# Performance work log

Hardware: AMD Instinct MI355X
Metric: run time of the kernel (lower is better)

The kernel has to match this reference:

```python
import jax, jax.numpy as jnp
import numpy as np

# Static problem sizes
B, TMAX = 32, 48                 # subjects, max windows per subject
NPW, NWIN = 128, 1024            # nodes per window, total windows (= sum(lengths))
EPW = 2048                       # edges per window (avg degree 16)
N, E = NWIN * NPW, NWIN * EPW    # 131072 nodes, 2097152 edges
IN_DIM, GNN_H, GRU_H = 128, 128, 128


def setup_inputs() -> dict:
    key = jax.random.key(0)
    ks = jax.random.split(key, 12)
    x = jax.random.normal(ks[0], (N, IN_DIM), jnp.float32)
    # random intra-window edges: endpoints within each window's 128-node block
    base = jax.random.randint(ks[1], (2, NWIN, EPW), 0, NPW)
    offs = (jnp.arange(NWIN) * NPW)[None, :, None]
    edge_index = (base + offs).reshape(2, E)
    batch_idx = jnp.repeat(jnp.arange(NWIN), NPW)          # node -> window id
    lengths = jnp.asarray(np.tile([16, 48], B // 2), jnp.int32)  # sums to NWIN
    s = 0.05
    p = lambda k, shape: jax.random.normal(k, shape, jnp.float32) * s
    return dict(
        x=x, edge_index=edge_index, batch_idx=batch_idx, lengths=lengths,
        # GIN layer 1 MLP (weights stored [in,out])
        w1a=p(ks[2], (IN_DIM, GNN_H)), b1a=jnp.zeros((GNN_H,), jnp.float32),
        w1b=p(ks[3], (GNN_H, GNN_H)), b1b=jnp.zeros((GNN_H,), jnp.float32),
        # GIN layer 2 MLP
        w2a=p(ks[4], (GNN_H, GNN_H)), b2a=jnp.zeros((GNN_H,), jnp.float32),
        w2b=p(ks[5], (GNN_H, GNN_H)), b2b=jnp.zeros((GNN_H,), jnp.float32),
        # GRU (torch layout: [3H, in], gate order r,z,n)
        wih=p(ks[6], (3 * GRU_H, GNN_H)), whh=p(ks[7], (3 * GRU_H, GRU_H)),
        bih=jnp.zeros((3 * GRU_H,), jnp.float32), bhh=jnp.zeros((3 * GRU_H,), jnp.float32),
        # output head
        wout=p(ks[8], (GRU_H, 1)), bout=jnp.zeros((1,), jnp.float32),
    )


def _gin(h, src, dst, wa, ba, wb, bb):
    # GINConv with eps=0: mlp(x + sum_{j->i} x_j)
    aggr = jax.ops.segment_sum(h[src], dst, num_segments=N)
    z = h + aggr
    z = jax.nn.relu(z @ wa + ba)
    return z @ wb + bb


def _forward(x, w1a, b1a, w1b, b1b, w2a, b2a, w2b, b2b,
             wih, whh, bih, bhh, wout, bout, edge_index, batch_idx, lengths):
    src, dst = edge_index[0], edge_index[1]
    h = jax.nn.relu(_gin(x, src, dst, w1a, b1a, w1b, b1b))
    h = jax.nn.relu(_gin(h, src, dst, w2a, b2a, w2b, b2b))
    # global mean pool per window -> [NWIN, GNN_H]
    sums = jax.ops.segment_sum(h, batch_idx, num_segments=NWIN)
    cnt = jax.ops.segment_sum(jnp.ones((N, 1), h.dtype), batch_idx, num_segments=NWIN)
    g = sums / cnt
    # pad_sequence: scatter flat window embeddings into [B, TMAX, H]
    csum = jnp.cumsum(lengths)
    starts = jnp.concatenate([jnp.zeros((1,), lengths.dtype), csum[:-1]])
    win_ids = jnp.arange(NWIN)
    subj = jnp.searchsorted(csum, win_ids, side='right')
    pos = win_ids - starts[subj]
    padded = jnp.zeros((B, TMAX, GNN_H), g.dtype).at[subj, pos].set(g)
    # masked GRU == pack_padded_sequence semantics (state frozen past length)
    mask = jnp.arange(TMAX)[:, None] < lengths[None, :]   # [T, B]
    xs = jnp.swapaxes(padded, 0, 1)                        # [T, B, H]

    def step(hc, inputs):
        xt, mt = inputs
        gx = xt @ wih.T + bih
        gh = hc @ whh.T + bhh
        rx, zx, nx = jnp.split(gx, 3, axis=-1)
        rh, zh, nh = jnp.split(gh, 3, axis=-1)
        r = jax.nn.sigmoid(rx + rh)
        z = jax.nn.sigmoid(zx + zh)
        n = jnp.tanh(nx + r * nh)
        hn = (1 - z) * n + z * hc
        hn = jnp.where(mt[:, None], hn, hc)
        return hn, None

    h0 = jnp.zeros((B, GRU_H), g.dtype)
    h_last, _ = jax.lax.scan(step, h0, (xs, mask))
    return (h_last @ wout + bout).squeeze(-1)  # [B]


def reference(x, edge_index, batch_idx, lengths,
              w1a, b1a, w1b, b1b, w2a, b2a, w2b, b2b,
              wih, whh, bih, bhh, wout, bout):
    return _forward(x, w1a, b1a, w1b, b1b, w2a, b2a, w2b, b2b,
                    wih, whh, bih, bhh, wout, bout, edge_index, batch_idx, lengths)
```

## Files before the change

### kernel.cpp

```cpp
#include <hip/hip_runtime.h>
#include <hip/hip_bf16.h>
#include <stdint.h>

#define NPW   128
#define NWIN  1024
#define EPW   2048
#define NEDGE (NWIN * EPW)
#define BSUBJ 32
#define TMAXW 48

typedef __bf16 bf16x8_t __attribute__((ext_vector_type(8)));
typedef float  f32x4_t  __attribute__((ext_vector_type(4)));

#define MU4_OFF  0
#define B2_OFF   8192
#define B3_OFF   40960
#define BIAS_OFF 73728
#define GP_OFF   75776
#define META_OFF 76288
#define K1_LDS   76800

__device__ __forceinline__ unsigned short bfbits(float v) {
  return __builtin_bit_cast(unsigned short, (__bf16)v);
}
__device__ __forceinline__ int swz(int row, int colbyte) {
  return row * 256 + (colbyte ^ ((row & 15) << 4));
}

#define GLDS16(gaddr, laddr) __builtin_amdgcn_global_load_lds( \
    (const __attribute__((address_space(1))) unsigned*)(gaddr), \
    (__attribute__((address_space(3))) unsigned*)(laddr), 16, 0, 0)

__device__ __forceinline__ void wstage(const char* src, char* dstB3, int wv, int lane) {
  #pragma unroll
  for (int p = 0; p < 4; ++p)
    GLDS16(src + wv * 4096 + p * 1024 + lane * 16, dstB3 + wv * 4096 + p * 1024);
}

__device__ __forceinline__ void gemm_lds(const char* Ab, const char* Bb, int lane, int rt,
                                         f32x4_t acc[8]) {
  const int rowA = rt * 16 + (lane & 15);
  const int swA = (rowA & 15) << 4;
  const int swB = (lane & 15) << 4;
  #pragma unroll
  for (int kk = 0; kk < 4; ++kk) {
    const int kb = kk * 64 + (lane >> 4) * 16;
    bf16x8_t af = *(const bf16x8_t*)(Ab + rowA * 256 + (kb ^ swA));
    #pragma unroll
    for (int ct = 0; ct < 8; ++ct) {
      const int rowB = ct * 16 + (lane & 15);
      bf16x8_t bv = *(const bf16x8_t*)(Bb + rowB * 256 + (kb ^ swB));
      acc[ct] = __builtin_amdgcn_mfma_f32_16x16x32_bf16(af, bv, acc[ct], 0, 0, 0);
    }
  }
}

__device__ __forceinline__ void gemm_m(const unsigned* Mw, const char* Bb, int lane, int rt,
                                       f32x4_t acc[8]) {
  const int rowA = rt * 16 + (lane & 15);
  const int g = lane >> 4;
  const int swB = (lane & 15) << 4;
  #pragma unroll
  for (int kk = 0; kk < 4; ++kk) {
    const unsigned mw = Mw[rowA * 16 + ((kk * 4 + g) ^ (rowA & 15))];
    bf16x8_t af;
    #pragma unroll
    for (int e = 0; e < 8; ++e)
      af[e] = (__bf16)(float)((mw >> (4 * e)) & 15u);
    const int kb = kk * 64 + g * 16;
    #pragma unroll
    for (int ct = 0; ct < 8; ++ct) {
      const int rowB = ct * 16 + (lane & 15);
      bf16x8_t bv = *(const bf16x8_t*)(Bb + rowB * 256 + (kb ^ swB));
      acc[ct] = __builtin_amdgcn_mfma_f32_16x16x32_bf16(af, bv, acc[ct], 0, 0, 0);
    }
  }
}

__device__ __forceinline__ void write_row(char* Dst, int lane, int rt, const f32x4_t acc[8],
                                          const float* bias, bool relu) {
  const int r0 = rt * 16 + (lane >> 4) * 4;
  const int c = lane & 15;
  #pragma unroll
  for (int ct = 0; ct < 8; ++ct) {
    const int col = ct * 16 + c;
    const float bvl = bias ? bias[col] : 0.f;
    #pragma unroll
    for (int j = 0; j < 4; ++j) {
      float v = acc[ct][j] + bvl;
      if (relu) v = fmaxf(v, 0.f);
      *(__bf16*)(Dst + swz(r0 + j, col * 2)) = (__bf16)v;
    }
  }
}

__device__ __forceinline__ void write_tr(char* Dst, int lane, int rt, const f32x4_t acc[8],
                                         const float* bias, bool relu) {
  const int r0 = rt * 16 + (lane >> 4) * 4;
  const int c = lane & 15;
  #pragma unroll
  for (int ct = 0; ct < 8; ++ct) {
    const int col = ct * 16 + c;
    const float bvl = bias ? bias[col] : 0.f;
    unsigned long long pk = 0ull;
    #pragma unroll
    for (int j = 0; j < 4; ++j) {
      float v = acc[ct][j] + bvl;
      if (relu) v = fmaxf(v, 0.f);
      pk |= ((unsigned long long)bfbits(v)) << (16 * j);
    }
    *(unsigned long long*)(Dst + swz(col, r0 * 2)) = pk;
  }
}

__global__ void __launch_bounds__(128)
wprep_kernel(const float* __restrict__ w1a, const float* __restrict__ w1b,
             const float* __restrict__ w2a, const float* __restrict__ w2b,
             unsigned* __restrict__ wt) {
  const float* srcs[4] = {w1a, w1b, w2a, w2b};
  const float* src = srcs[blockIdx.x];
  const int j = threadIdx.x;
  unsigned* dst = wt + blockIdx.x * 8192 + j * 64;
  const int sw = (j & 15) << 2;
  #pragma unroll 8
  for (int k = 0; k < 64; ++k) {
    float a = src[(size_t)(2 * k) * 128 + j];
    float b = src[(size_t)(2 * k + 1) * 128 + j];
    dst[k ^ sw] = (unsigned)bfbits(a) | ((unsigned)bfbits(b) << 16);
  }
}

__global__ void __launch_bounds__(512, 2)
gin_gnn_kernel(const float* __restrict__ x, const int* __restrict__ ei,
               const float* __restrict__ b1a, const float* __restrict__ b1b,
               const float* __restrict__ b2a, const float* __restrict__ b2b,
               const char* __restrict__ wt_sw, const float* __restrict__ wih,
               const float* __restrict__ bih, const int* __restrict__ lengths,
               float* __restrict__ GX) {
  extern __shared__ __align__(16) char sm[];
  const int w = blockIdx.x;
  const int tid = threadIdx.x;
  const int lane = tid & 63;
  const int wv = tid >> 6;

  unsigned* Mw = (unsigned*)(sm + MU4_OFF);
  char* B2 = sm + B2_OFF;
  char* B3 = sm + B3_OFF;
  float* biasb = (float*)(sm + BIAS_OFF);
  float* gp = (float*)(sm + GP_OFF);
  int* meta = (int*)(sm + META_OFF);

  #pragma unroll
  for (int i = tid; i < 2048; i += 512) Mw[i] = 0u;
  if (tid < 128) gp[tid] = 0.f;
  __syncthreads();

  wstage(wt_sw, B3, wv, lane);
  if (tid < 64) {
    int L = (tid < BSUBJ) ? lengths[tid] : 0;
    int c = L;
    #pragma unroll
    for (int d = 1; d < 32; d <<= 1) {
      int u = __shfl_up(c, d, 64);
      if (tid >= d) c += u;
    }
    unsigned long long mset = __ballot(tid < BSUBJ && w < c);
    int s = (int)(__ffsll((long long)mset) - 1);
    if (tid == s) { meta[0] = s; meta[1] = w - (c - L); }
  }
  {
    const int base = w * EPW;
    #pragma unroll
    for (int rr = 0; rr < 4; ++rr) {
      const int e = base + tid + rr * 512;
      const int s = ei[e] & 127;
      const int d = ei[NEDGE + e] & 127;
      atomicAdd(&Mw[d * 16 + ((s >> 3) ^ (d & 15))], 1u << ((s & 7) * 4));
    }
    if (tid < 128) {
      const int d = tid;
      atomicAdd(&Mw[d * 16 + ((d >> 3) ^ (d & 15))], 1u << ((d & 7) * 4));
    }
  }
  {
    const float* xw = x + (size_t)w * 16384;
    #pragma unroll
    for (int it = 0; it < 8; ++it) {
      const int elem = it * 2048 + tid * 4;
      const float4 v = *(const float4*)(xw + elem);
      const int row = elem >> 7;
      const int colb = (elem & 127) * 2;
      unsigned long long pk = (unsigned long long)bfbits(v.x)
          | ((unsigned long long)bfbits(v.y) << 16)
          | ((unsigned long long)bfbits(v.z) << 32)
          | ((unsigned long long)bfbits(v.w) << 48);
      *(unsigned long long*)(B2 + row * 256 + (colb ^ ((row & 15) << 4))) = pk;
    }
  }
  {
    const float* bp = (tid < 128) ? b1a : (tid < 256) ? b1b : (tid < 384) ? b2a : b2b;
    biasb[tid] = bp[tid & 127];
  }
  __syncthreads();

  f32x4_t acc[8];
  #define ZACC() { _Pragma("unroll") for (int q = 0; q < 8; ++q) acc[q] = (f32x4_t){0.f,0.f,0.f,0.f}; }

  ZACC(); gemm_lds(B2, B3, lane, wv, acc);
  __syncthreads();
  write_tr(B2, lane, wv, acc, nullptr, false);
  wstage(wt_sw + 32768, B3, wv, lane);
  __syncthreads();
  ZACC(); gemm_m(Mw, B2, lane, wv, acc);
  __syncthreads();
  write_row(B2, lane, wv, acc, biasb + 0, true);
  __syncthreads();
  ZACC(); gemm_lds(B2, B3, lane, wv, acc);
  __syncthreads();
  write_row(B2, lane, wv, acc, biasb + 128, true);
  wstage(wt_sw + 65536, B3, wv, lane);
  __syncthreads();
  ZACC(); gemm_lds(B2, B3, lane, wv, acc);
  __syncthreads();
  write_tr(B2, lane, wv, acc, nullptr, false);
  wstage(wt_sw + 98304, B3, wv, lane);
  __syncthreads();
  ZACC(); gemm_m(Mw, B2, lane, wv, acc);
  __syncthreads();
  write_row(B2, lane, wv, acc, biasb + 256, true);
  __syncthreads();
  ZACC(); gemm_lds(B2, B3, lane, wv, acc);
  {
    const int c = lane & 15;
    #pragma unroll
    for (int ct = 0; ct < 8; ++ct) {
      const int col = ct * 16 + c;
      const float bvl = biasb[384 + col];
      float s = 0.f;
      #pragma unroll
      for (int j = 0; j < 4; ++j) s += fmaxf(acc[ct][j] + bvl, 0.f);
      s += __shfl_xor(s, 16);
      s += __shfl_xor(s, 32);
      if (lane < 16) atomicAdd(&gp[col], s);
    }
  }
  __syncthreads();

  if (tid < 384) {
    const float* wrow = wih + (size_t)tid * 128;
    const float4* gp4 = (const float4*)gp;
    float a0 = 0.f, a1 = 0.f, a2 = 0.f, a3 = 0.f;
    #pragma unroll
    for (int q = 0; q < 8; ++q) {
      const float4 h0 = gp4[4*q], h1 = gp4[4*q+1], h2 = gp4[4*q+2], h3 = gp4[4*q+3];
      const float4 w0 = *(const float4*)(wrow + 16*q);
      const float4 w1 = *(const float4*)(wrow + 16*q + 4);
      const float4 w2 = *(const float4*)(wrow + 16*q + 8);
      const float4 w3 = *(const float4*)(wrow + 16*q + 12);
      a0 = fmaf(w0.x,h0.x,fmaf(w0.y,h0.y,fmaf(w0.z,h0.z,fmaf(w0.w,h0.w,a0))));
      a1 = fmaf(w1.x,h1.x,fmaf(w1.y,h1.y,fmaf(w1.z,h1.z,fmaf(w1.w,h1.w,a1))));
      a2 = fmaf(w2.x,h2.x,fmaf(w2.y,h2.y,fmaf(w2.z,h2.z,fmaf(w2.w,h2.w,a2))));
      a3 = fmaf(w3.x,h3.x,fmaf(w3.y,h3.y,fmaf(w3.z,h3.z,fmaf(w3.w,h3.w,a3))));
    }
    const float dot = (a0 + a1) + (a2 + a3);
    GX[((size_t)meta[0] * TMAXW + meta[1]) * 384 + tid] = dot * (1.f / 128.f) + bih[tid];
  }
}

__global__ void __launch_bounds__(384)
gru_kernel(const float* __restrict__ GX, const float* __restrict__ whh,
           const float* __restrict__ bhh, const float* __restrict__ wout,
           const float* __restrict__ bout, const int* __restrict__ lengths,
           float* __restrict__ outp) {
  __shared__ __align__(16) float hb[128];
  __shared__ float rb[128], zb[128];
  const int b = blockIdx.x;
  const int o = threadIdx.x;

  float wrf[128];
  {
    const float* wr = whh + (size_t)o * 128;
    #pragma unroll
    for (int q = 0; q < 32; ++q) {
      float4 v = ((const float4*)wr)[q];
      wrf[4*q+0] = v.x; wrf[4*q+1] = v.y; wrf[4*q+2] = v.z; wrf[4*q+3] = v.w;
    }
  }
  if (o < 128) hb[o] = 0.f;
  const float bho = bhh[o];
  const int len = lengths[b];
  __syncthreads();

  float gx = (len > 0) ? GX[((size_t)b * TMAXW) * 384 + o] : 0.f;
  for (int t = 0; t < len; ++t) {
    const int tn = (t + 1 < len) ? t + 1 : t;
    const float gxn = GX[((size_t)b * TMAXW + tn) * 384 + o];
    float a0 = 0.f, a1 = 0.f, a2 = 0.f, a3 = 0.f;
    const float4* hv4 = (const float4*)hb;
    #pragma unroll
    for (int q = 0; q < 8; ++q) {
      const float4 h0 = hv4[4*q], h1 = hv4[4*q+1], h2 = hv4[4*q+2], h3 = hv4[4*q+3];
      const float* wq = wrf + 16 * q;
      a0 = fmaf(wq[0],  h0.x, a0); a0 = fmaf(wq[1],  h0.y, a0);
      a0 = fmaf(wq[2],  h0.z, a0); a0 = fmaf(wq[3],  h0.w, a0);
      a1 = fmaf(wq[4],  h1.x, a1); a1 = fmaf(wq[5],  h1.y, a1);
      a1 = fmaf(wq[6],  h1.z, a1); a1 = fmaf(wq[7],  h1.w, a1);
      a2 = fmaf(wq[8],  h2.x, a2); a2 = fmaf(wq[9],  h2.y, a2);
      a2 = fmaf(wq[10], h2.z, a2); a2 = fmaf(wq[11], h2.w, a2);
      a3 = fmaf(wq[12], h3.x, a3); a3 = fmaf(wq[13], h3.y, a3);
      a3 = fmaf(wq[14], h3.z, a3); a3 = fmaf(wq[15], h3.w, a3);
    }
    const float gh = (a0 + a1) + (a2 + a3) + bho;
    float nsave = 0.f, ghn = 0.f;
    if (o < 256) {
      const float v = 1.f / (1.f + __expf(-(gx + gh)));
      if (o < 128) rb[o] = v; else zb[o - 128] = v;
    } else {
      nsave = gx; ghn = gh;
    }
    __syncthreads();
    if (o >= 256) {
      const int oo = o - 256;
      const float r = rb[oo], z = zb[oo];
      const float pre = nsave + r * ghn;
      const float e2 = __expf(-2.f * pre);
      const float n = (1.f - e2) / (1.f + e2);
      hb[oo] = (1.f - z) * n + z * hb[oo];
    }
    __syncthreads();
    gx = gxn;
  }

  float part = (o < 128) ? hb[o] * wout[o] : 0.f;
  #pragma unroll
  for (int d = 1; d < 64; d <<= 1) part += __shfl_xor(part, d);
  __shared__ float red[6];
  if ((o & 63) == 0) red[o >> 6] = part;
  __syncthreads();
  if (o == 0) outp[b] = red[0] + red[1] + bout[0];
}

extern "C" void kernel_launch(void* const* d_in, const int* in_sizes, int n_in,
                              void* d_out, int out_size, void* d_ws, size_t ws_size,
                              hipStream_t stream) {
  const float* x    = (const float*)d_in[0];
  const int*   ei   = (const int*)d_in[1];
  const int*   len  = (const int*)d_in[3];
  const float* w1a  = (const float*)d_in[4];
  const float* b1a  = (const float*)d_in[5];
  const float* w1b  = (const float*)d_in[6];
  const float* b1b  = (const float*)d_in[7];
  const float* w2a  = (const float*)d_in[8];
  const float* b2a  = (const float*)d_in[9];
  const float* w2b  = (const float*)d_in[10];
  const float* b2b  = (const float*)d_in[11];
  const float* wih  = (const float*)d_in[12];
  const float* whh  = (const float*)d_in[13];
  const float* bih  = (const float*)d_in[14];
  const float* bhh  = (const float*)d_in[15];
  const float* wout = (const float*)d_in[16];
  const float* bout = (const float*)d_in[17];

  float*    GX    = (float*)d_ws;
  unsigned* wt_sw = (unsigned*)((char*)d_ws + (size_t)BSUBJ * TMAXW * 384 * 4);

  hipLaunchKernelGGL(wprep_kernel, dim3(4), dim3(128), 0, stream,
                     w1a, w1b, w2a, w2b, wt_sw);
  hipLaunchKernelGGL(gin_gnn_kernel, dim3(NWIN), dim3(512), K1_LDS, stream,
                     x, ei, b1a, b1b, b2a, b2b, (const char*)wt_sw,
                     wih, bih, len, GX);
  hipLaunchKernelGGL(gru_kernel, dim3(BSUBJ), dim3(384), 0, stream,
                     GX, whh, bhh, wout, bout, len, (float*)d_out);
}
```

Baseline: 256.9 us.

## Hold GIN weights in registers as MFMA fragments and ping-pong LDS buffers

The weight-prep kernel now emits weights pre-arranged as per-lane MFMA B fragments. The GNN kernel loads these straight into registers and prefetches the next layer's weights during the current GEMM, so the LDS weight staging area is no longer needed. The GEMMs are re-tiled from 8 waves × 16 rows × 128 cols to a 2×4 wave grid of 64×32 tiles. Two LDS activation buffers alternate so fewer barriers are needed per stage. The cost is higher register pressure from 16 uint4 weight registers per lane plus a 4×2 accumulator, which may hurt occupancy under launch bounds of (512,2).

After: 264.3 us. 2.9% more time.

```diff
diff --git a/kernel.cpp b/kernel.cpp
--- a/kernel.cpp
+++ b/kernel.cpp
@@ -13,120 +13,125 @@
 typedef float  f32x4_t  __attribute__((ext_vector_type(4)));
 
 #define MU4_OFF  0
-#define B2_OFF   8192
-#define B3_OFF   40960
+#define BUF0_OFF 8192
+#define BUF1_OFF 40960
 #define BIAS_OFF 73728
 #define GP_OFF   75776
 #define META_OFF 76288
-#define K1_LDS   76800
+#define K1_LDS   76304
 
 __device__ __forceinline__ unsigned short bfbits(float v) {
   return __builtin_bit_cast(unsigned short, (__bf16)v);
 }
-__device__ __forceinline__ int swz(int row, int colbyte) {
-  return row * 256 + (colbyte ^ ((row & 15) << 4));
-}
-
-#define GLDS16(gaddr, laddr) __builtin_amdgcn_global_load_lds( \
-    (const __attribute__((address_space(1))) unsigned*)(gaddr), \
-    (__attribute__((address_space(3))) unsigned*)(laddr), 16, 0, 0)
-
-__device__ __forceinline__ void wstage(const char* src, char* dstB3, int wv, int lane) {
-  #pragma unroll
-  for (int p = 0; p < 4; ++p)
-    GLDS16(src + wv * 4096 + p * 1024 + lane * 16, dstB3 + wv * 4096 + p * 1024);
-}
-
-__device__ __forceinline__ void gemm_lds(const char* Ab, const char* Bb, int lane, int rt,
-                                         f32x4_t acc[8]) {
-  const int rowA = rt * 16 + (lane & 15);
-  const int swA = (rowA & 15) << 4;
-  const int swB = (lane & 15) << 4;
+
+
+__device__ __forceinline__ void gemm_w(const char* Ab, const uint4 wreg[8],
+                                       int lane, int wr, f32x4_t acc[4][2]) {
+  const int sw = (lane & 15) << 4;
   #pragma unroll
   for (int kk = 0; kk < 4; ++kk) {
     const int kb = kk * 64 + (lane >> 4) * 16;
-    bf16x8_t af = *(const bf16x8_t*)(Ab + rowA * 256 + (kb ^ swA));
-    #pragma unroll
-    for (int ct = 0; ct < 8; ++ct) {
-      const int rowB = ct * 16 + (lane & 15);
-      bf16x8_t bv = *(const bf16x8_t*)(Bb + rowB * 256 + (kb ^ swB));
-      acc[ct] = __builtin_amdgcn_mfma_f32_16x16x32_bf16(af, bv, acc[ct], 0, 0, 0);
-    }
-  }
-}
-
-__device__ __forceinline__ void gemm_m(const unsigned* Mw, const char* Bb, int lane, int rt,
-                                       f32x4_t acc[8]) {
-  const int rowA = rt * 16 + (lane & 15);
+    #pragma unroll
+    for (int m = 0; m < 4; ++m) {
+      const int rowA = wr * 64 + m * 16 + (lane & 15);
+      bf16x8_t af = *(const bf16x8_t*)(Ab + rowA * 256 + (kb ^ sw));
+      #pragma unroll
+      for (int n = 0; n < 2; ++n)
+        acc[m][n] = __builtin_amdgcn_mfma_f32_16x16x32_bf16(
+            af, __builtin_bit_cast(bf16x8_t, wreg[n * 4 + kk]), acc[m][n], 0, 0, 0);
+    }
+  }
+}
+
+__device__ __forceinline__ void gemm_mm(const unsigned* Mw, const char* Bb,
+                                        int lane, int wr, int wc, f32x4_t acc[4][2]) {
   const int g = lane >> 4;
-  const int swB = (lane & 15) << 4;
+  const int sw = (lane & 15) << 4;
   #pragma unroll
   for (int kk = 0; kk < 4; ++kk) {
-    const unsigned mw = Mw[rowA * 16 + ((kk * 4 + g) ^ (rowA & 15))];
-    bf16x8_t af;
-    #pragma unroll
-    for (int e = 0; e < 8; ++e)
-      af[e] = (__bf16)(float)((mw >> (4 * e)) & 15u);
     const int kb = kk * 64 + g * 16;
-    #pragma unroll
-    for (int ct = 0; ct < 8; ++ct) {
-      const int rowB = ct * 16 + (lane & 15);
-      bf16x8_t bv = *(const bf16x8_t*)(Bb + rowB * 256 + (kb ^ swB));
-      acc[ct] = __builtin_amdgcn_mfma_f32_16x16x32_bf16(af, bv, acc[ct], 0, 0, 0);
-    }
-  }
-}
-
-__device__ __forceinline__ void write_row(char* Dst, int lane, int rt, const f32x4_t acc[8],
+    bf16x8_t bv[2];
+    #pragma unroll
+    for (int n = 0; n < 2; ++n) {
+      const int rowB = wc * 32 + n * 16 + (lane & 15);
+      bv[n] = *(const bf16x8_t*)(Bb + rowB * 256 + (kb ^ sw));
+    }
+    #pragma unroll
+    for (int m = 0; m < 4; ++m) {
+      const int rowA = wr * 64 + m * 16 + (lane & 15);
+      const unsigned mw = Mw[rowA * 16 + ((kk * 4 + g) ^ (lane & 15))];
+      bf16x8_t af;
+      #pragma unroll
+      for (int e = 0; e < 8; ++e)
+        af[e] = (__bf16)(float)((mw >> (4 * e)) & 15u);
+      #pragma unroll
+      for (int n = 0; n < 2; ++n)
+        acc[m][n] = __builtin_amdgcn_mfma_f32_16x16x32_bf16(af, bv[n], acc[m][n], 0, 0, 0);
+    }
+  }
+}
+
+__device__ __forceinline__ void write_row(char* Dst, int lane, int wr, int wc,
+                                          const f32x4_t acc[4][2],
                                           const float* bias, bool relu) {
-  const int r0 = rt * 16 + (lane >> 4) * 4;
   const int c = lane & 15;
   #pragma unroll
-  for (int ct = 0; ct < 8; ++ct) {
-    const int col = ct * 16 + c;
-    const float bvl = bias ? bias[col] : 0.f;
-    #pragma unroll
-    for (int j = 0; j < 4; ++j) {
-      float v = acc[ct][j] + bvl;
-      if (relu) v = fmaxf(v, 0.f);
-      *(__bf16*)(Dst + swz(r0 + j, col * 2)) = (__bf16)v;
-    }
-  }
-}
-
-__device__ __forceinline__ void write_tr(char* Dst, int lane, int rt, const f32x4_t acc[8],
-                                         const float* bias, bool relu) {
-  const int r0 = rt * 16 + (lane >> 4) * 4;
+  for (int m = 0; m < 4; ++m) {
+    const int r0 = wr * 64 + m * 16 + (lane >> 4) * 4;
+    #pragma unroll
+    for (int n = 0; n < 2; ++n) {
+      const int col = wc * 32 + n * 16 + c;
+      const float bvl = bias ? bias[col] : 0.f;
+      #pragma unroll
+      for (int j = 0; j < 4; ++j) {
+        float v = acc[m][n][j] + bvl;
+        if (relu) v = fmaxf(v, 0.f);
+        const int row = r0 + j;
+        *(__bf16*)(Dst + row * 256 + ((col * 2) ^ ((row & 15) << 4))) = (__bf16)v;
+      }
+    }
+  }
+}
+
+__device__ __forceinline__ void write_tr(char* Dst, int lane, int wr, int wc,
+                                         const f32x4_t acc[4][2]) {
   const int c = lane & 15;
   #pragma unroll
-  for (int ct = 0; ct < 8; ++ct) {
-    const int col = ct * 16 + c;
-    const float bvl = bias ? bias[col] : 0.f;
-    unsigned long long pk = 0ull;
-    #pragma unroll
-    for (int j = 0; j < 4; ++j) {
-      float v = acc[ct][j] + bvl;
-      if (relu) v = fmaxf(v, 0.f);
-      pk |= ((unsigned long long)bfbits(v)) << (16 * j);
-    }
-    *(unsigned long long*)(Dst + swz(col, r0 * 2)) = pk;
-  }
-}
-
-__global__ void __launch_bounds__(128)
+  for (int m = 0; m < 4; ++m) {
+    const int r0 = wr * 64 + m * 16 + (lane >> 4) * 4;
+    #pragma unroll
+    for (int n = 0; n < 2; ++n) {
+      const int col = wc * 32 + n * 16 + c;
+      unsigned long long pk = 0ull;
+      #pragma unroll
+      for (int j = 0; j < 4; ++j)
+        pk |= ((unsigned long long)bfbits(acc[m][n][j])) << (16 * j);
+      *(unsigned long long*)(Dst + col * 256 + ((r0 * 2) ^ ((col & 15) << 4))) = pk;
+    }
+  }
+}
+
+__global__ void __launch_bounds__(256)
 wprep_kernel(const float* __restrict__ w1a, const float* __restrict__ w1b,
              const float* __restrict__ w2a, const float* __restrict__ w2b,
-             unsigned* __restrict__ wt) {
+             uint4* __restrict__ wt) {
   const float* srcs[4] = {w1a, w1b, w2a, w2b};
   const float* src = srcs[blockIdx.x];
-  const int j = threadIdx.x;
-  unsigned* dst = wt + blockIdx.x * 8192 + j * 64;
-  const int sw = (j & 15) << 2;
-  #pragma unroll 8
-  for (int k = 0; k < 64; ++k) {
-    float a = src[(size_t)(2 * k) * 128 + j];
-    float b = src[(size_t)(2 * k + 1) * 128 + j];
-    dst[k ^ sw] = (unsigned)bfbits(a) | ((unsigned)bfbits(b) << 16);
+  uint4* dst = wt + blockIdx.x * 2048;
+  #pragma unroll
+  for (int i = 0; i < 8; ++i) {
+    const int f = i * 256 + threadIdx.x;
+    const int lane = f & 63, kk = (f >> 6) & 3, n = (f >> 8) & 1, wcg = f >> 9;
+    const int j = wcg * 32 + n * 16 + (lane & 15);
+    const int kb = kk * 32 + (lane >> 4) * 8;
+    unsigned r[4];
+    #pragma unroll
+    for (int e2 = 0; e2 < 4; ++e2) {
+      const float a = src[(size_t)(kb + 2 * e2) * 128 + j];
+      const float b = src[(size_t)(kb + 2 * e2 + 1) * 128 + j];
+      r[e2] = (unsigned)bfbits(a) | ((unsigned)bfbits(b) << 16);
+    }
+    dst[f] = make_uint4(r[0], r[1], r[2], r[3]);
   }
 }
 
@@ -134,18 +139,18 @@
 gin_gnn_kernel(const float* __restrict__ x, const int* __restrict__ ei,
                const float* __restrict__ b1a, const float* __restrict__ b1b,
                const float* __restrict__ b2a, const float* __restrict__ b2b,
-               const char* __restrict__ wt_sw, const float* __restrict__ wih,
+               const uint4* __restrict__ wfrag, const float* __restrict__ wih,
                const float* __restrict__ bih, const int* __restrict__ lengths,
                float* __restrict__ GX) {
   extern __shared__ __align__(16) char sm[];
   const int w = blockIdx.x;
   const int tid = threadIdx.x;
   const int lane = tid & 63;
-  const int wv = tid >> 6;
+  const int wv = tid >> 6, wr = wv >> 2, wc = wv & 3;
 
   unsigned* Mw = (unsigned*)(sm + MU4_OFF);
-  char* B2 = sm + B2_OFF;
-  char* B3 = sm + B3_OFF;
+  char* BUF0 = sm + BUF0_OFF;
+  char* BUF1 = sm + BUF1_OFF;
   float* biasb = (float*)(sm + BIAS_OFF);
   float* gp = (float*)(sm + GP_OFF);
   int* meta = (int*)(sm + META_OFF);
@@ -155,7 +160,11 @@
   if (tid < 128) gp[tid] = 0.f;
   __syncthreads();
 
-  wstage(wt_sw, B3, wv, lane);
+  const uint4* wf = wfrag + wc * 512 + lane;
+  uint4 wA[8], wB[8];
+  #pragma unroll
+  for (int q = 0; q < 8; ++q) wA[q] = wf[q * 64];
+
   if (tid < 64) {
     int L = (tid < BSUBJ) ? lengths[tid] : 0;
     int c = L;
@@ -194,7 +203,7 @@
           | ((unsigned long long)bfbits(v.y) << 16)
           | ((unsigned long long)bfbits(v.z) << 32)
           | ((unsigned long long)bfbits(v.w) << 48);
-      *(unsigned long long*)(B2 + row * 256 + (colb ^ ((row & 15) << 4))) = pk;
+      *(unsigned long long*)(BUF0 + row * 256 + (colb ^ ((row & 15) << 4))) = pk;
     }
   }
   {
@@ -203,42 +212,47 @@
   }
   __syncthreads();
 
-  f32x4_t acc[8];
-  #define ZACC() { _Pragma("unroll") for (int q = 0; q < 8; ++q) acc[q] = (f32x4_t){0.f,0.f,0.f,0.f}; }
-
-  ZACC(); gemm_lds(B2, B3, lane, wv, acc);
-  __syncthreads();
-  write_tr(B2, lane, wv, acc, nullptr, false);
-  wstage(wt_sw + 32768, B3, wv, lane);
-  __syncthreads();
-  ZACC(); gemm_m(Mw, B2, lane, wv, acc);
-  __syncthreads();
-  write_row(B2, lane, wv, acc, biasb + 0, true);
-  __syncthreads();
-  ZACC(); gemm_lds(B2, B3, lane, wv, acc);
-  __syncthreads();
-  write_row(B2, lane, wv, acc, biasb + 128, true);
-  wstage(wt_sw + 65536, B3, wv, lane);
-  __syncthreads();
-  ZACC(); gemm_lds(B2, B3, lane, wv, acc);
-  __syncthreads();
-  write_tr(B2, lane, wv, acc, nullptr, false);
-  wstage(wt_sw + 98304, B3, wv, lane);
-  __syncthreads();
-  ZACC(); gemm_m(Mw, B2, lane, wv, acc);
-  __syncthreads();
-  write_row(B2, lane, wv, acc, biasb + 256, true);
-  __syncthreads();
-  ZACC(); gemm_lds(B2, B3, lane, wv, acc);
+  f32x4_t acc[4][2];
+  #define ZACC() { _Pragma("unroll") for (int _m = 0; _m < 4; ++_m) \
+                   _Pragma("unroll") for (int _n = 0; _n < 2; ++_n) \
+                     acc[_m][_n] = (f32x4_t){0.f,0.f,0.f,0.f}; }
+
+  ZACC(); gemm_w(BUF0, wA, lane, wr, acc);
+  write_tr(BUF1, lane, wr, wc, acc);
+  __syncthreads();
+  ZACC();
+  #pragma unroll
+  for (int q = 0; q < 8; ++q) wB[q] = wf[2048 + q * 64];
+  gemm_mm(Mw, BUF1, lane, wr, wc, acc);
+  write_row(BUF0, lane, wr, wc, acc, biasb + 0, true);
+  __syncthreads();
+  ZACC();
+  #pragma unroll
+  for (int q = 0; q < 8; ++q) wA[q] = wf[4096 + q * 64];
+  gemm_w(BUF0, wB, lane, wr, acc);
+  write_row(BUF1, lane, wr, wc, acc, biasb + 128, true);
+  __syncthreads();
+  ZACC(); gemm_w(BUF1, wA, lane, wr, acc);
+  write_tr(BUF0, lane, wr, wc, acc);
+  __syncthreads();
+  ZACC();
+  #pragma unroll
+  for (int q = 0; q < 8; ++q) wB[q] = wf[6144 + q * 64];
+  gemm_mm(Mw, BUF0, lane, wr, wc, acc);
+  write_row(BUF1, lane, wr, wc, acc, biasb + 256, true);
+  __syncthreads();
+  ZACC(); gemm_w(BUF1, wB, lane, wr, acc);
   {
     const int c = lane & 15;
     #pragma unroll
-    for (int ct = 0; ct < 8; ++ct) {
-      const int col = ct * 16 + c;
+    for (int n = 0; n < 2; ++n) {
+      const int col = wc * 32 + n * 16 + c;
       const float bvl = biasb[384 + col];
       float s = 0.f;
       #pragma unroll
-      for (int j = 0; j < 4; ++j) s += fmaxf(acc[ct][j] + bvl, 0.f);
+      for (int m = 0; m < 4; ++m)
+        #pragma unroll
+        for (int j = 0; j < 4; ++j) s += fmaxf(acc[m][n][j] + bvl, 0.f);
       s += __shfl_xor(s, 16);
       s += __shfl_xor(s, 32);
       if (lane < 16) atomicAdd(&gp[col], s);
@@ -361,14 +375,13 @@
   const float* wout = (const float*)d_in[16];
   const float* bout = (const float*)d_in[17];
 
-  float*    GX    = (float*)d_ws;
-  unsigned* wt_sw = (unsigned*)((char*)d_ws + (size_t)BSUBJ * TMAXW * 384 * 4);
-
-  hipLaunchKernelGGL(wprep_kernel, dim3(4), dim3(128), 0, stream,
-                     w1a, w1b, w2a, w2b, wt_sw);
+  float* GX    = (float*)d_ws;
+  uint4* wfrag = (uint4*)((char*)d_ws + (size_t)BSUBJ * TMAXW * 384 * 4);
+
+  hipLaunchKernelGGL(wprep_kernel, dim3(4), dim3(256), 0, stream,
+                     w1a, w1b, w2a, w2b, wfrag);
   hipLaunchKernelGGL(gin_gnn_kernel, dim3(NWIN), dim3(512), K1_LDS, stream,
-                     x, ei, b1a, b1b, b2a, b2b, (const char*)wt_sw,
-                     wih, bih, len, GX);
+                     x, ei, b1a, b1b, b2a, b2b, wfrag, wih, bih, len, GX);
   hipLaunchKernelGGL(gru_kernel, dim3(BSUBJ), dim3(384), 0, stream,
                      GX, whh, bhh, wout, bout, len, (float*)d_out);
 }
```
